# Kernel tuning notes

Hardware: AMD Instinct MI355X
Metric: run time of the kernel (lower is better)

Reference implementation:

```python
import jax, jax.numpy as jnp
import numpy as np

N_HEADS = 4
LN_EPS = 1e-12


def _ln(x, g, b):
    mu = jnp.mean(x, axis=-1, keepdims=True)
    var = jnp.var(x, axis=-1, keepdims=True)
    return (x - mu) * jax.lax.rsqrt(var + LN_EPS) * g + b


def _mha(q_in, kv_in, qkv_w, qkv_b, o_w, o_b):
    # q_in: [B,Sq,H], kv_in: [B,Sk,H]; qkv_w: [3,H,H], qkv_b: [3,H]
    B, Sq, H = q_in.shape
    Sk = kv_in.shape[1]
    hd = H // N_HEADS
    q = (q_in @ qkv_w[0] + qkv_b[0]).reshape(B, Sq, N_HEADS, hd)
    k = (kv_in @ qkv_w[1] + qkv_b[1]).reshape(B, Sk, N_HEADS, hd)
    v = (kv_in @ qkv_w[2] + qkv_b[2]).reshape(B, Sk, N_HEADS, hd)
    scale = 1.0 / jnp.sqrt(jnp.asarray(hd, q_in.dtype))
    scores = jnp.einsum('bqhd,bkhd->bhqk', q, k) * scale  # [B,H,Sq,Sk]
    probs = jax.nn.softmax(scores, axis=-1)
    ctx = jnp.einsum('bhqk,bkhd->bqhd', probs, v).reshape(B, Sq, H)
    return ctx @ o_w + o_b


def reference(x, y, pos_embed, self_qkv_w, self_qkv_b, self_o_w, self_o_b,
              cross_qkv_w, cross_qkv_b, cross_o_w, cross_o_b,
              ffn_w1, ffn_b1, ffn_w2, ffn_b2, ln_g, ln_b):
    # positional embedding added to encoder sequence
    x = x + pos_embed[: x.shape[1]][None]
    h = y
    n_layers = self_qkv_w.shape[0]
    for i in range(n_layers):  # 6 structurally-identical decoder layers
        a = _mha(h, h, self_qkv_w[i], self_qkv_b[i], self_o_w[i], self_o_b[i])
        h = _ln(h + a, ln_g[i, 0], ln_b[i, 0])
        c = _mha(h, x, cross_qkv_w[i], cross_qkv_b[i], cross_o_w[i], cross_o_b[i])
        h = _ln(h + c, ln_g[i, 1], ln_b[i, 1])
        f = jax.nn.gelu(h @ ffn_w1[i] + ffn_b1[i]) @ ffn_w2[i] + ffn_b2[i]
        h = _ln(h + f, ln_g[i, 2], ln_b[i, 2])
    return h


def setup_inputs() -> dict:
    key = jax.random.key(0)
    ks = jax.random.split(key, 12)
    B, Se, Sd, H, L, F = 2, 4096, 2048, 256, 6, 1024
    s = 0.02  # weight init scale
    return {
        'x': jax.random.normal(ks[0], (B, Se, H), jnp.float32),
        'y': jax.random.normal(ks[1], (B, Sd, H), jnp.float32),
        'pos_embed': jax.random.normal(ks[2], (4096, H), jnp.float32) * s,
        'self_qkv_w': jax.random.normal(ks[3], (L, 3, H, H), jnp.float32) * s,
        'self_qkv_b': jnp.zeros((L, 3, H), jnp.float32),
        'self_o_w': jax.random.normal(ks[4], (L, H, H), jnp.float32) * s,
        'self_o_b': jnp.zeros((L, H), jnp.float32),
        'cross_qkv_w': jax.random.normal(ks[5], (L, 3, H, H), jnp.float32) * s,
        'cross_qkv_b': jnp.zeros((L, 3, H), jnp.float32),
        'cross_o_w': jax.random.normal(ks[6], (L, H, H), jnp.float32) * s,
        'cross_o_b': jnp.zeros((L, H), jnp.float32),
        'ffn_w1': jax.random.normal(ks[7], (L, H, F), jnp.float32) * s,
        'ffn_b1': jnp.zeros((L, F), jnp.float32),
        'ffn_w2': jax.random.normal(ks[8], (L, F, H), jnp.float32) * s,
        'ffn_b2': jnp.zeros((L, H), jnp.float32),
        'ln_g': jnp.ones((L, 3, H), jnp.float32),
        'ln_b': jnp.zeros((L, 3, H), jnp.float32),
    }
```

## Files before the change

kernel.cpp:

```cpp
#include <hip/hip_runtime.h>
#include <hip/hip_bf16.h>

typedef unsigned short u16;
typedef __attribute__((ext_vector_type(8))) short bhalf8;
typedef __attribute__((ext_vector_type(4))) short bhalf4;
typedef __attribute__((ext_vector_type(4))) float f32x4;

__device__ inline f32x4 mfma_bf16(bhalf8 a, bhalf8 b, f32x4 c) {
    return __builtin_amdgcn_mfma_f32_16x16x32_bf16(a, b, c, 0, 0, 0);
}
__device__ inline f32x4 mfma16_bf16(bhalf4 a, bhalf4 b, f32x4 c) {
    return __builtin_amdgcn_mfma_f32_16x16x16bf16_1k(a, b, c, 0, 0, 0);
}

__device__ inline u16 f2bf(float f) {
    union { float f; unsigned u; } v; v.f = f;
    unsigned u = v.u;
    return (u16)((u + 0x7fff + ((u >> 16) & 1)) >> 16);
}
__device__ inline unsigned pkbf(float lo_, float hi_) {
    return ((unsigned)f2bf(hi_) << 16) | (unsigned)f2bf(lo_);
}
__device__ inline unsigned pk2bf(float lo, float hi) {
    union { __hip_bfloat162 h; unsigned u; } v;
    v.h = __float22bfloat162_rn(float2{lo, hi});
    return v.u;
}

__device__ inline size_t afm_off(int row, int col, int Cc) {
    return ((size_t)((row >> 4) * Cc + (col >> 5))) * 512
         + (((row & 15) + 16 * ((col >> 3) & 3)) << 3) + (col & 7);
}


__global__ __launch_bounds__(256) void k_wtrans_fm(const float* in, u16* out, int rows, int cols) {
    int mat = blockIdx.y;
    size_t rc = (size_t)rows * cols;
    size_t idx = (size_t)blockIdx.x * 256 + threadIdx.x;
    if (idx >= rc) return;
    int r = (int)(idx / cols), c = (int)(idx % cols);
    size_t off = ((size_t)((c >> 4) * (rows >> 5) + (r >> 5))) * 512
               + (((c & 15) + 16 * ((r >> 3) & 3)) << 3) + (r & 7);
    out[mat * rc + off] = f2bf(in[mat * rc + idx]);
}

__global__ __launch_bounds__(256) void k_addpos(const float* x, const float* pos, u16* xp) {
    size_t idx = (size_t)blockIdx.x * 256 + threadIdx.x;
    size_t p = idx & ((size_t)4096 * 256 - 1);
    int row = (int)(idx >> 8), col = (int)(idx & 255);
    xp[afm_off(row, col, 8)] = f2bf(x[idx] + pos[p]);
}

__global__ __launch_bounds__(256) void k_inith(const float* y, float* h, u16* hb) {
    size_t idx = (size_t)blockIdx.x * 256 + threadIdx.x;
    float v = y[idx];
    h[idx] = v;
    int row = (int)(idx >> 8), col = (int)(idx & 255);
    hb[afm_off(row, col, 8)] = f2bf(v);
}

__global__ __launch_bounds__(256) void k_kv_pre(const u16* A2, const u16* Wall, const float* ball,
                                                u16* kfm_all, u16* vfm_all) {
    const int Skv = 4096;
    int layer = blockIdx.z;
    int wave = threadIdx.x >> 6, lane = threadIdx.x & 63;
    int l16 = lane & 15, quad = lane >> 4;
    int row0 = blockIdx.x * 64 + wave * 16;
    int col0 = blockIdx.y * 32;
    const u16* Wk = Wall + (size_t)layer * 3 * 65536 + 65536;
    const u16* Wv = Wk + 65536;
    const float* bk = ball + layer * 768 + 256;
    const float* bv = bk + 256;
    u16* kout = kfm_all + (size_t)layer * 2097152;
    u16* vout = vfm_all + (size_t)layer * 2097152;
    const int Kc = 8;

    f32x4 acck0 = (f32x4){0.f, 0.f, 0.f, 0.f};
    f32x4 acck1 = (f32x4){0.f, 0.f, 0.f, 0.f};
    f32x4 accv0 = (f32x4){0.f, 0.f, 0.f, 0.f};
    f32x4 accv1 = (f32x4){0.f, 0.f, 0.f, 0.f};
    const u16* ab  = A2 + (size_t)(row0 >> 4) * Kc * 512 + lane * 8;
    const u16* wk0 = Wk + (size_t)(col0 >> 4) * Kc * 512 + lane * 8;
    const u16* wk1 = wk0 + (size_t)Kc * 512;
    const u16* wv0 = Wv + (size_t)(col0 >> 4) * Kc * 512 + lane * 8;
    const u16* wv1 = wv0 + (size_t)Kc * 512;
    #pragma unroll
    for (int kc = 0; kc < Kc; kc++) {
        bhalf8 a = *(const bhalf8*)(ab + kc * 512);
        acck0 = mfma_bf16(a, *(const bhalf8*)(wk0 + kc * 512), acck0);
        acck1 = mfma_bf16(a, *(const bhalf8*)(wk1 + kc * 512), acck1);
        accv0 = mfma_bf16(a, *(const bhalf8*)(wv0 + kc * 512), accv0);
        accv1 = mfma_bf16(a, *(const bhalf8*)(wv1 + kc * 512), accv1);
    }

    {
        f32x4 accs[2] = {acck0, acck1};
        #pragma unroll
        for (int nt = 0; nt < 2; nt++) {
            int col = col0 + nt * 16 + l16;
            float bs = bk[col];
            int hh = col >> 6, dim = col & 63;
            int f = dim >> 5, q8 = (dim >> 3) & 3, i8 = dim & 7;
            #pragma unroll
            for (int r = 0; r < 4; r++) {
                int row = row0 + quad * 4 + r;
                int bb = row / Skv; int key = row - bb * Skv;
                size_t off = (size_t)(bb * 4 + hh) * Skv * 64 + (size_t)(key >> 4) * 1024
                           + f * 512 + q8 * 128 + (key & 15) * 8 + i8;
                kout[off] = f2bf(accs[nt][r] + bs);
            }
        }
    }
    {
        f32x4 accs[2] = {accv0, accv1};
        #pragma unroll
        for (int nt = 0; nt < 2; nt++) {
            int col = col0 + nt * 16 + l16;
            float bs = bv[col];
            int hh = col >> 6, dim = col & 63;
            int ntg = dim >> 4, l16v = dim & 15;
            int row = row0 + quad * 4;
            int bb = row / Skv; int key = row - bb * Skv;
            size_t off = (size_t)(bb * 4 + hh) * Skv * 64 + (size_t)(key >> 4) * 1024
                       + ntg * 256 + ((key & 15) >> 2) * 64 + l16v * 4;
            ushort4 pk;
            pk.x = f2bf(accs[nt][0] + bs);
            pk.y = f2bf(accs[nt][1] + bs);
            pk.z = f2bf(accs[nt][2] + bs);
            pk.w = f2bf(accs[nt][3] + bs);
            *(ushort4*)(vout + off) = pk;
        }
    }
}

__global__ __launch_bounds__(256) void k_gemm_qkv(const u16* A0, const u16* A2,
                                                  const u16* Wfm0, const float* bias0,
                                                  u16* qout, u16* kfm_out, u16* vfm_out,
                                                  int K, long wz, long bz, float scale0,
                                                  int kz, int vz, int Skv, int M0) {
    int z = blockIdx.z;
    int wave = threadIdx.x >> 6, lane = threadIdx.x & 63;
    int l16 = lane & 15, quad = lane >> 4;
    int row0 = blockIdx.x * 64 + wave * 16;
    int col0 = blockIdx.y * 32;
    const u16* A;
    if (z == 0) { if (row0 >= M0) return; A = A0; } else { A = A2; }
    const u16* Wfm = Wfm0 + (size_t)z * wz;
    const float* bias = bias0 + (size_t)z * bz;
    int Kc = K >> 5;

    f32x4 acc0 = (f32x4){0.f, 0.f, 0.f, 0.f};
    f32x4 acc1 = (f32x4){0.f, 0.f, 0.f, 0.f};
    const u16* ab = A + (size_t)(row0 >> 4) * Kc * 512 + lane * 8;
    const u16* wb0 = Wfm + (size_t)(col0 >> 4) * Kc * 512 + lane * 8;
    const u16* wb1 = wb0 + (size_t)Kc * 512;
    #pragma unroll 4
    for (int kc = 0; kc < Kc; kc++) {
        bhalf8 a = *(const bhalf8*)(ab + kc * 512);
        acc0 = mfma_bf16(a, *(const bhalf8*)(wb0 + kc * 512), acc0);
        acc1 = mfma_bf16(a, *(const bhalf8*)(wb1 + kc * 512), acc1);
    }

    f32x4 accs[2] = {acc0, acc1};
    #pragma unroll
    for (int nt = 0; nt < 2; nt++) {
        int col = col0 + nt * 16 + l16;
        float bs = bias[col];
        if (z == kz) {
            int hh = col >> 6, dim = col & 63;
            int f = dim >> 5, q8 = (dim >> 3) & 3, i8 = dim & 7;
            #pragma unroll
            for (int r = 0; r < 4; r++) {
                int row = row0 + quad * 4 + r;
                int bb = row / Skv; int key = row - bb * Skv;
                size_t off = (size_t)(bb * 4 + hh) * Skv * 64 + (size_t)(key >> 4) * 1024
                           + f * 512 + q8 * 128 + (key & 15) * 8 + i8;
                kfm_out[off] = f2bf(accs[nt][r] + bs);
            }
        } else if (z == vz) {
            int hh = col >> 6, dim = col & 63;
            int ntg = dim >> 4, l16v = dim & 15;
            int row = row0 + quad * 4;
            int bb = row / Skv; int key = row - bb * Skv;
            size_t off = (size_t)(bb * 4 + hh) * Skv * 64 + (size_t)(key >> 4) * 1024
                       + ntg * 256 + ((key & 15) >> 2) * 64 + l16v * 4;
            ushort4 pk;
            pk.x = f2bf(accs[nt][0] + bs);
            pk.y = f2bf(accs[nt][1] + bs);
            pk.z = f2bf(accs[nt][2] + bs);
            pk.w = f2bf(accs[nt][3] + bs);
            *(ushort4*)(vfm_out + off) = pk;
        } else {
            size_t base = ((size_t)(row0 >> 4) * 8 + blockIdx.y) * 512;
            int g3 = (nt * 2 + (l16 >> 3)) & 3;
            int i = l16 & 7;
            #pragma unroll
            for (int r = 0; r < 4; r++)
                qout[base + (((quad * 4 + r) + 16 * g3) << 3) + i] =
                    f2bf((accs[nt][r] + bs) * scale0);
        }
    }
}

__global__ __launch_bounds__(512) void k_gemm_ln(const u16* A, const u16* Wfm, const float* bias,
                                                 const float* res, const float* g, const float* beta,
                                                 float* outf, u16* outb, int K) {
    int t = threadIdx.x;
    int w = t >> 6, lane = t & 63;
    int l16 = lane & 15, quad = lane >> 4;
    int row0 = blockIdx.x * 16;
    int Kc = K >> 5;

    f32x4 acc[2];
    acc[0] = (f32x4){0.f, 0.f, 0.f, 0.f};
    acc[1] = (f32x4){0.f, 0.f, 0.f, 0.f};

    const u16* ab = A + (size_t)blockIdx.x * Kc * 512 + lane * 8;
    const u16* wb = Wfm + (size_t)(w * 2) * Kc * 512 + lane * 8;
    #pragma unroll 4
    for (int kc = 0; kc < Kc; kc++) {
        bhalf8 a = *(const bhalf8*)(ab + kc * 512);
        acc[0] = mfma_bf16(a, *(const bhalf8*)(wb + kc * 512), acc[0]);
        acc[1] = mfma_bf16(a, *(const bhalf8*)(wb + (size_t)(Kc + kc) * 512), acc[1]);
    }

    float sr[4] = {0.f, 0.f, 0.f, 0.f}, s2r[4] = {0.f, 0.f, 0.f, 0.f};
    #pragma unroll
    for (int nt = 0; nt < 2; nt++) {
        int col = w * 32 + nt * 16 + l16;
        float bs = bias[col];
        #pragma unroll
        for (int r = 0; r < 4; r++) {
            int row = row0 + quad * 4 + r;
            float v = acc[nt][r] + bs + res[(size_t)row * 256 + col];
            acc[nt][r] = v;
            sr[r] += v; s2r[r] += v * v;
        }
    }
    #pragma unroll
    for (int r = 0; r < 4; r++) {
        #pragma unroll
        for (int off = 8; off >= 1; off >>= 1) {
            sr[r]  += __shfl_xor(sr[r], off, 16);
            s2r[r] += __shfl_xor(s2r[r], off, 16);
        }
    }
    __shared__ float lsm[8][16], lsq[8][16];
    if (l16 == 0) {
        #pragma unroll
        for (int r = 0; r < 4; r++) { lsm[w][quad * 4 + r] = sr[r]; lsq[w][quad * 4 + r] = s2r[r]; }
    }
    __syncthreads();
    float mu[4], rs[4];
    #pragma unroll
    for (int r = 0; r < 4; r++) {
        int ri = quad * 4 + r;
        float ts = 0.f, tq = 0.f;
        #pragma unroll
        for (int ww = 0; ww < 8; ww++) { ts += lsm[ww][ri]; tq += lsq[ww][ri]; }
        mu[r] = ts * (1.f / 256.f);
        float var = tq * (1.f / 256.f) - mu[r] * mu[r];
        rs[r] = rsqrtf(var + 1e-12f);
    }
    size_t base = ((size_t)blockIdx.x * 8 + w) * 512;
    #pragma unroll
    for (int nt = 0; nt < 2; nt++) {
        int col = w * 32 + nt * 16 + l16;
        float gc = g[col], bc = beta[col];
        int g3 = (nt * 2 + (l16 >> 3)) & 3;
        int i = l16 & 7;
        #pragma unroll
        for (int r = 0; r < 4; r++) {
            int row = row0 + quad * 4 + r;
            float yv = (acc[nt][r] - mu[r]) * rs[r] * gc + bc;
            outf[(size_t)row * 256 + col] = yv;
            outb[base + (((quad * 4 + r) + 16 * g3) << 3) + i] = f2bf(yv);
        }
    }
}

__global__ __launch_bounds__(512) void k_ffn(const u16* A, const u16* W1, const float* b1,
                                             const u16* W2, const float* b2,
                                             const float* res, const float* g, const float* beta,
                                             float* outf, u16* outb) {
    int t = threadIdx.x;
    int w = t >> 6, lane = t & 63;
    int l16 = lane & 15, quad = lane >> 4;
    int row0 = blockIdx.x * 16;

    __shared__ u16 f1lds[32 * 512];
    __shared__ float lsm[8][16], lsq[8][16];

    f32x4 acc[8];
    #pragma unroll
    for (int nt = 0; nt < 8; nt++) acc[nt] = (f32x4){0.f, 0.f, 0.f, 0.f};
    const u16* ab = A + (size_t)blockIdx.x * 8 * 512 + lane * 8;
    const u16* w1b = W1 + (size_t)(w * 8) * 8 * 512 + lane * 8;
    #pragma unroll
    for (int kc = 0; kc < 8; kc++) {
        bhalf8 a = *(const bhalf8*)(ab + kc * 512);
        #pragma unroll
        for (int nt = 0; nt < 8; nt++)
            acc[nt] = mfma_bf16(a, *(const bhalf8*)(w1b + ((size_t)nt * 8 + kc) * 512), acc[nt]);
    }
    #pragma unroll
    for (int nt = 0; nt < 8; nt++) {
        int col = w * 128 + nt * 16 + l16;
        float bs = b1[col];
        int chunk = w * 4 + (nt >> 1);
        int g3 = (nt * 2 + (l16 >> 3)) & 3;
        int i = l16 & 7;
        #pragma unroll
        for (int r = 0; r < 4; r++) {
            float v = acc[nt][r] + bs;
            float ge = 0.5f * v * (1.f + tanhf(0.7978845608028654f * (v + 0.044715f * v * v * v)));
            f1lds[chunk * 512 + (((quad * 4 + r) + 16 * g3) << 3) + i] = f2bf(ge);
        }
    }
    __syncthreads();

    f32x4 acc2[2];
    acc2[0] = (f32x4){0.f, 0.f, 0.f, 0.f};
    acc2[1] = (f32x4){0.f, 0.f, 0.f, 0.f};
    const u16* w2b = W2 + (size_t)(w * 2) * 32 * 512 + lane * 8;
    #pragma unroll 4
    for (int kc = 0; kc < 32; kc++) {
        bhalf8 a = *(const bhalf8*)&f1lds[kc * 512 + lane * 8];
        acc2[0] = mfma_bf16(a, *(const bhalf8*)(w2b + (size_t)kc * 512), acc2[0]);
        acc2[1] = mfma_bf16(a, *(const bhalf8*)(w2b + (size_t)(32 + kc) * 512), acc2[1]);
    }

    float sr[4] = {0.f, 0.f, 0.f, 0.f}, s2r[4] = {0.f, 0.f, 0.f, 0.f};
    #pragma unroll
    for (int nt = 0; nt < 2; nt++) {
        int col = w * 32 + nt * 16 + l16;
        float bs = b2[col];
        #pragma unroll
        for (int r = 0; r < 4; r++) {
            int row = row0 + quad * 4 + r;
            float v = acc2[nt][r] + bs + res[(size_t)row * 256 + col];
            acc2[nt][r] = v;
            sr[r] += v; s2r[r] += v * v;
        }
    }
    #pragma unroll
    for (int r = 0; r < 4; r++) {
        #pragma unroll
        for (int off = 8; off >= 1; off >>= 1) {
            sr[r]  += __shfl_xor(sr[r], off, 16);
            s2r[r] += __shfl_xor(s2r[r], off, 16);
        }
    }
    if (l16 == 0) {
        #pragma unroll
        for (int r = 0; r < 4; r++) { lsm[w][quad * 4 + r] = sr[r]; lsq[w][quad * 4 + r] = s2r[r]; }
    }
    __syncthreads();
    float mu[4], rs[4];
    #pragma unroll
    for (int r = 0; r < 4; r++) {
        int ri = quad * 4 + r;
        float ts = 0.f, tq = 0.f;
        #pragma unroll
        for (int ww = 0; ww < 8; ww++) { ts += lsm[ww][ri]; tq += lsq[ww][ri]; }
        mu[r] = ts * (1.f / 256.f);
        float var = tq * (1.f / 256.f) - mu[r] * mu[r];
        rs[r] = rsqrtf(var + 1e-12f);
    }
    size_t base = ((size_t)blockIdx.x * 8 + w) * 512;
    #pragma unroll
    for (int nt = 0; nt < 2; nt++) {
        int col = w * 32 + nt * 16 + l16;
        float gc = g[col], bc = beta[col];
        int g3 = (nt * 2 + (l16 >> 3)) & 3;
        int i = l16 & 7;
        #pragma unroll
        for (int r = 0; r < 4; r++) {
            int row = row0 + quad * 4 + r;
            float yv = (acc2[nt][r] - mu[r]) * rs[r] * gc + bc;
            outf[(size_t)row * 256 + col] = yv;
            outb[base + (((quad * 4 + r) + 16 * g3) << 3) + i] = f2bf(yv);
        }
    }
}

__global__ __launch_bounds__(512, 4) void k_attn(const u16* q, const u16* kfm, const u16* vfm,
                                                 u16* ctx, int Sq, int Sk) {
    int bh = blockIdx.x & 7;
    int b = bh >> 2, h = bh & 3;
    int qp = blockIdx.x >> 3;
    int t = threadIdx.x;
    int kw = t >> 6, lane = t & 63;
    int l16 = lane & 15, quad = lane >> 4;
    int q0 = qp * 32;

    __shared__ float opart[2][7][64][20];
    __shared__ float lsum[2][7][16];

    size_t rt0 = (size_t)((b * Sq + q0) >> 4);
    const u16* qb = q + (rt0 * 8 + h * 2) * 512 + lane * 8;
    bhalf8 bq00 = *(const bhalf8*)(qb);
    bhalf8 bq01 = *(const bhalf8*)(qb + 512);
    bhalf8 bq10 = *(const bhalf8*)(qb + 8 * 512);
    bhalf8 bq11 = *(const bhalf8*)(qb + 9 * 512);

    const u16* kwb = kfm + (size_t)(b * 4 + h) * Sk * 64;
    const u16* vwb = vfm + (size_t)(b * 4 + h) * Sk * 64;

    int nT = Sk >> 7;
    int T0 = kw * nT;

    float l0 = 0.f, l1 = 0.f;
    f32x4 o0[4], o1[4];
    #pragma unroll
    for (int nt = 0; nt < 4; nt++) {
        o0[nt] = (f32x4){0.f, 0.f, 0.f, 0.f};
        o1[nt] = (f32x4){0.f, 0.f, 0.f, 0.f};
    }

    #pragma unroll 2
    for (int T = T0; T < T0 + nT; T++) {
        const u16* kt = kwb + (size_t)T * 1024;
        bhalf8 a0 = *(const bhalf8*)(kt + lane * 8);
        bhalf8 a1 = *(const bhalf8*)(kt + 512 + lane * 8);
        f32x4 s0 = (f32x4){0.f, 0.f, 0.f, 0.f};
        f32x4 s1 = (f32x4){0.f, 0.f, 0.f, 0.f};
        s0 = mfma_bf16(a0, bq00, s0);
        s0 = mfma_bf16(a1, bq01, s0);
        s1 = mfma_bf16(a0, bq10, s1);
        s1 = mfma_bf16(a1, bq11, s1);

        float p0[4], p1[4], ps0 = 0.f, ps1 = 0.f;
        #pragma unroll
        for (int r = 0; r < 4; r++) {
            p0[r] = exp2f(s0[r] - 11.5415603f);
            ps0 += p0[r];
            p1[r] = exp2f(s1[r] - 11.5415603f);
            ps1 += p1[r];
        }
        l0 += ps0; l1 += ps1;

        union { bhalf4 v; unsigned u[2]; } bp0, bp1;
        bp0.u[0] = pk2bf(p0[0], p0[1]);
        bp0.u[1] = pk2bf(p0[2], p0[3]);
        bp1.u[0] = pk2bf(p1[0], p1[1]);
        bp1.u[1] = pk2bf(p1[2], p1[3]);

        const u16* vts = vwb + (size_t)T * 1024 + quad * 64 + l16 * 4;
        #pragma unroll
        for (int nt = 0; nt < 4; nt++) {
            bhalf4 va = *(const bhalf4*)(vts + nt * 256);
            o0[nt] = mfma16_bf16(va, bp0.v, o0[nt]);
            o1[nt] = mfma16_bf16(va, bp1.v, o1[nt]);
        }
    }

    float lc0 = l0, lc1 = l1;
    lc0 += __shfl_xor(lc0, 16, 64);
    lc0 += __shfl_xor(lc0, 32, 64);
    lc1 += __shfl_xor(lc1, 16, 64);
    lc1 += __shfl_xor(lc1, 32, 64);

    if (kw > 0) {
        #pragma unroll
        for (int nt = 0; nt < 4; nt++)
            #pragma unroll
            for (int r = 0; r < 4; r++) {
                opart[0][kw - 1][nt * 16 + quad * 4 + r][l16] = o0[nt][r];
                opart[1][kw - 1][nt * 16 + quad * 4 + r][l16] = o1[nt][r];
            }
        if (quad == 0) {
            lsum[0][kw - 1][l16] = lc0;
            lsum[1][kw - 1][l16] = lc1;
        }
    }
    __syncthreads();
    if (kw == 0) {
        float L0 = lc0, L1 = lc1;
        #pragma unroll
        for (int ww = 0; ww < 7; ww++) {
            L0 += lsum[0][ww][l16];
            L1 += lsum[1][ww][l16];
        }
        float invL0 = 1.f / L0;
        float invL1 = 1.f / L1;
        #pragma unroll
        for (int nt = 0; nt < 4; nt++) {
            ushort4 pkv0, pkv1;
            #pragma unroll
            for (int r = 0; r < 4; r++) {
                float v0 = o0[nt][r];
                float v1 = o1[nt][r];
                #pragma unroll
                for (int ww = 0; ww < 7; ww++) {
                    v0 += opart[0][ww][nt * 16 + quad * 4 + r][l16];
                    v1 += opart[1][ww][nt * 16 + quad * 4 + r][l16];
                }
                ((u16*)&pkv0)[r] = f2bf(v0 * invL0);
                ((u16*)&pkv1)[r] = f2bf(v1 * invL1);
            }
            size_t ce = ((l16 + 16 * ((nt * 2 + (quad >> 1)) & 3)) << 3) + (quad & 1) * 4;
            size_t off0 = (rt0 * 8 + (h * 2 + (nt >> 1))) * 512 + ce;
            size_t off1 = ((rt0 + 1) * 8 + (h * 2 + (nt >> 1))) * 512 + ce;
            *(ushort4*)(ctx + off0) = pkv0;
            *(ushort4*)(ctx + off1) = pkv1;
        }
    }
}

extern "C" void kernel_launch(void* const* d_in, const int* in_sizes, int n_in,
                              void* d_out, int out_size, void* d_ws, size_t ws_size,
                              hipStream_t stream) {
    const float* x        = (const float*)d_in[0];
    const float* y        = (const float*)d_in[1];
    const float* pos      = (const float*)d_in[2];
    const float* sqkv_w   = (const float*)d_in[3];
    const float* sqkv_b   = (const float*)d_in[4];
    const float* so_w     = (const float*)d_in[5];
    const float* so_b     = (const float*)d_in[6];
    const float* cqkv_w   = (const float*)d_in[7];
    const float* cqkv_b   = (const float*)d_in[8];
    const float* co_w     = (const float*)d_in[9];
    const float* co_b     = (const float*)d_in[10];
    const float* ffn_w1   = (const float*)d_in[11];
    const float* ffn_b1   = (const float*)d_in[12];
    const float* ffn_w2   = (const float*)d_in[13];
    const float* ffn_b2   = (const float*)d_in[14];
    const float* ln_g     = (const float*)d_in[15];
    const float* ln_b     = (const float*)d_in[16];

    char* w = (char*)d_ws;
    auto alloc = [&](size_t bytes) { char* p = w; w += (bytes + 255) & ~(size_t)255; return p; };

    u16* wt_sqkv = (u16*)alloc(18ull * 65536 * 2);
    u16* wt_so   = (u16*)alloc(6ull  * 65536 * 2);
    u16* wt_cqkv = (u16*)alloc(18ull * 65536 * 2);
    u16* wt_co   = (u16*)alloc(6ull  * 65536 * 2);
    u16* wt_f1   = (u16*)alloc(6ull  * 262144 * 2);
    u16* wt_f2   = (u16*)alloc(6ull  * 262144 * 2);
    u16* xp      = (u16*)alloc(2097152ull * 2);
    float* hf    = (float*)alloc(1048576ull * 4);
    u16* hb      = (u16*)alloc(1048576ull * 2);
    u16* qbuf    = (u16*)alloc(1048576ull * 2);
    u16* kfm     = (u16*)alloc(2097152ull * 2);
    u16* vfm     = (u16*)alloc(2097152ull * 2);
    u16* ctx     = (u16*)alloc(1048576ull * 2);
    u16* kfm_all = (u16*)alloc(6ull * 2097152 * 2);
    u16* vfm_all = (u16*)alloc(6ull * 2097152 * 2);

    k_wtrans_fm<<<dim3(256, 18), 256, 0, stream>>>(sqkv_w, wt_sqkv, 256, 256);
    k_wtrans_fm<<<dim3(256, 6),  256, 0, stream>>>(so_w,   wt_so,   256, 256);
    k_wtrans_fm<<<dim3(256, 18), 256, 0, stream>>>(cqkv_w, wt_cqkv, 256, 256);
    k_wtrans_fm<<<dim3(256, 6),  256, 0, stream>>>(co_w,   wt_co,   256, 256);
    k_wtrans_fm<<<dim3(1024, 6), 256, 0, stream>>>(ffn_w1, wt_f1,   256, 1024);
    k_wtrans_fm<<<dim3(1024, 6), 256, 0, stream>>>(ffn_w2, wt_f2,   1024, 256);
    k_addpos<<<dim3(8192), 256, 0, stream>>>(x, pos, xp);
    k_inith<<<dim3(4096), 256, 0, stream>>>(y, hf, hb);
    k_kv_pre<<<dim3(128, 8, 6), 256, 0, stream>>>(xp, wt_cqkv, cqkv_b, kfm_all, vfm_all);

    const float qscale = 0.125f * 1.44269504f;

    for (int i = 0; i < 6; i++) {
        k_gemm_qkv<<<dim3(64, 8, 3), 256, 0, stream>>>(hb, hb,
            wt_sqkv + (size_t)i * 3 * 65536, sqkv_b + i * 768,
            qbuf, kfm, vfm, 256, 65536, 256, qscale, 1, 2, 2048, 4096);
        k_attn<<<dim3(512), 512, 0, stream>>>(qbuf, kfm, vfm, ctx, 2048, 2048);
        k_gemm_ln<<<dim3(256), 512, 0, stream>>>(ctx, wt_so + (size_t)i * 65536,
            so_b + i * 256, hf, ln_g + (i * 3 + 0) * 256, ln_b + (i * 3 + 0) * 256,
            hf, hb, 256);

        k_gemm_qkv<<<dim3(64, 8, 1), 256, 0, stream>>>(hb, xp,
            wt_cqkv + (size_t)i * 3 * 65536, cqkv_b + i * 768,
            qbuf, kfm, vfm, 256, 65536, 256, qscale, 1, 2, 4096, 4096);
        k_attn<<<dim3(512), 512, 0, stream>>>(qbuf,
            kfm_all + (size_t)i * 2097152, vfm_all + (size_t)i * 2097152, ctx, 2048, 4096);
        k_gemm_ln<<<dim3(256), 512, 0, stream>>>(ctx, wt_co + (size_t)i * 65536,
            co_b + i * 256, hf, ln_g + (i * 3 + 1) * 256, ln_b + (i * 3 + 1) * 256,
            hf, hb, 256);

        float* dst = (i == 5) ? (float*)d_out : hf;
        k_ffn<<<dim3(256), 512, 0, stream>>>(hb, wt_f1 + (size_t)i * 262144,
            ffn_b1 + i * 1024, wt_f2 + (size_t)i * 262144, ffn_b2 + i * 256,
            hf, ln_g + (i * 3 + 2) * 256, ln_b + (i * 3 + 2) * 256, dst, hb);
    }
}
```

Before: 863.7 us.

## Stage cross-attention K/V weights in LDS and enlarge k_kv_pre tiles

The precompute kernel for cross-attention K/V now loads a 64-column slice of the K and V weights into shared memory once per block. Each block then iterates over 4 row tiles of 64 rows and 2 column pairs, with A fragments held in registers. This replaces the earlier direct global loads of weights per 16x32 tile and cuts redundant weight traffic. The cost is 64KB of LDS per block and a 4x smaller grid, which lowers occupancy and parallelism in a kernel that runs only once.

```diff
diff --git a/kernel.cpp b/kernel.cpp
--- a/kernel.cpp
+++ b/kernel.cpp
@@ -65,8 +65,6 @@
     int layer = blockIdx.z;
     int wave = threadIdx.x >> 6, lane = threadIdx.x & 63;
     int l16 = lane & 15, quad = lane >> 4;
-    int row0 = blockIdx.x * 64 + wave * 16;
-    int col0 = blockIdx.y * 32;
     const u16* Wk = Wall + (size_t)layer * 3 * 65536 + 65536;
     const u16* Wv = Wk + 65536;
     const float* bk = ball + layer * 768 + 256;
@@ -75,60 +73,82 @@
     u16* vout = vfm_all + (size_t)layer * 2097152;
     const int Kc = 8;
 
-    f32x4 acck0 = (f32x4){0.f, 0.f, 0.f, 0.f};
-    f32x4 acck1 = (f32x4){0.f, 0.f, 0.f, 0.f};
-    f32x4 accv0 = (f32x4){0.f, 0.f, 0.f, 0.f};
-    f32x4 accv1 = (f32x4){0.f, 0.f, 0.f, 0.f};
-    const u16* ab  = A2 + (size_t)(row0 >> 4) * Kc * 512 + lane * 8;
-    const u16* wk0 = Wk + (size_t)(col0 >> 4) * Kc * 512 + lane * 8;
-    const u16* wk1 = wk0 + (size_t)Kc * 512;
-    const u16* wv0 = Wv + (size_t)(col0 >> 4) * Kc * 512 + lane * 8;
-    const u16* wv1 = wv0 + (size_t)Kc * 512;
-    #pragma unroll
-    for (int kc = 0; kc < Kc; kc++) {
-        bhalf8 a = *(const bhalf8*)(ab + kc * 512);
-        acck0 = mfma_bf16(a, *(const bhalf8*)(wk0 + kc * 512), acck0);
-        acck1 = mfma_bf16(a, *(const bhalf8*)(wk1 + kc * 512), acck1);
-        accv0 = mfma_bf16(a, *(const bhalf8*)(wv0 + kc * 512), accv0);
-        accv1 = mfma_bf16(a, *(const bhalf8*)(wv1 + kc * 512), accv1);
-    }
-
-    {
-        f32x4 accs[2] = {acck0, acck1};
-        #pragma unroll
-        for (int nt = 0; nt < 2; nt++) {
-            int col = col0 + nt * 16 + l16;
-            float bs = bk[col];
-            int hh = col >> 6, dim = col & 63;
-            int f = dim >> 5, q8 = (dim >> 3) & 3, i8 = dim & 7;
+    __shared__ u16 wlds[8 * 4096];
+    #pragma unroll
+    for (int c = 0; c < 8; c++) {
+        int cp = c >> 2, mat = (c >> 1) & 1, nt = c & 1;
+        const u16* s = (mat ? Wv : Wk)
+                     + (size_t)(((blockIdx.y * 64 + cp * 32) >> 4) + nt) * 4096;
+        *(bhalf8*)&wlds[c * 4096 + threadIdx.x * 16]     = *(const bhalf8*)(s + threadIdx.x * 16);
+        *(bhalf8*)&wlds[c * 4096 + threadIdx.x * 16 + 8] = *(const bhalf8*)(s + threadIdx.x * 16 + 8);
+    }
+    __syncthreads();
+
+    for (int rt = 0; rt < 4; rt++) {
+        int row0 = blockIdx.x * 256 + rt * 64 + wave * 16;
+        const u16* ab = A2 + (size_t)(row0 >> 4) * Kc * 512 + lane * 8;
+        bhalf8 af[8];
+        #pragma unroll
+        for (int kc = 0; kc < 8; kc++) af[kc] = *(const bhalf8*)(ab + kc * 512);
+
+        #pragma unroll
+        for (int cp = 0; cp < 2; cp++) {
+            int col0 = blockIdx.y * 64 + cp * 32;
+            const u16* lk0 = &wlds[(cp * 4 + 0) * 4096 + lane * 8];
+            const u16* lk1 = &wlds[(cp * 4 + 1) * 4096 + lane * 8];
+            const u16* lv0 = &wlds[(cp * 4 + 2) * 4096 + lane * 8];
+            const u16* lv1 = &wlds[(cp * 4 + 3) * 4096 + lane * 8];
+            f32x4 acck0 = (f32x4){0.f, 0.f, 0.f, 0.f};
+            f32x4 acck1 = (f32x4){0.f, 0.f, 0.f, 0.f};
+            f32x4 accv0 = (f32x4){0.f, 0.f, 0.f, 0.f};
+            f32x4 accv1 = (f32x4){0.f, 0.f, 0.f, 0.f};
             #pragma unroll
-            for (int r = 0; r < 4; r++) {
-                int row = row0 + quad * 4 + r;
-                int bb = row / Skv; int key = row - bb * Skv;
-                size_t off = (size_t)(bb * 4 + hh) * Skv * 64 + (size_t)(key >> 4) * 1024
-                           + f * 512 + q8 * 128 + (key & 15) * 8 + i8;
-                kout[off] = f2bf(accs[nt][r] + bs);
+            for (int kc = 0; kc < Kc; kc++) {
+                bhalf8 a = af[kc];
+                acck0 = mfma_bf16(a, *(const bhalf8*)(lk0 + kc * 512), acck0);
+                acck1 = mfma_bf16(a, *(const bhalf8*)(lk1 + kc * 512), acck1);
+                accv0 = mfma_bf16(a, *(const bhalf8*)(lv0 + kc * 512), accv0);
+                accv1 = mfma_bf16(a, *(const bhalf8*)(lv1 + kc * 512), accv1);
             }
-        }
-    }
-    {
-        f32x4 accs[2] = {accv0, accv1};
-        #pragma unroll
-        for (int nt = 0; nt < 2; nt++) {
-            int col = col0 + nt * 16 + l16;
-            float bs = bv[col];
-            int hh = col >> 6, dim = col & 63;
-            int ntg = dim >> 4, l16v = dim & 15;
-            int row = row0 + quad * 4;
-            int bb = row / Skv; int key = row - bb * Skv;
-            size_t off = (size_t)(bb * 4 + hh) * Skv * 64 + (size_t)(key >> 4) * 1024
-                       + ntg * 256 + ((key & 15) >> 2) * 64 + l16v * 4;
-            ushort4 pk;
-            pk.x = f2bf(accs[nt][0] + bs);
-            pk.y = f2bf(accs[nt][1] + bs);
-            pk.z = f2bf(accs[nt][2] + bs);
-            pk.w = f2bf(accs[nt][3] + bs);
-            *(ushort4*)(vout + off) = pk;
+
+            {
+                f32x4 accs[2] = {acck0, acck1};
+                #pragma unroll
+                for (int nt = 0; nt < 2; nt++) {
+                    int col = col0 + nt * 16 + l16;
+                    float bs = bk[col];
+                    int hh = col >> 6, dim = col & 63;
+                    int f = dim >> 5, q8 = (dim >> 3) & 3, i8 = dim & 7;
+                    #pragma unroll
+                    for (int r = 0; r < 4; r++) {
+                        int row = row0 + quad * 4 + r;
+                        int bb = row / Skv; int key = row - bb * Skv;
+                        size_t off = (size_t)(bb * 4 + hh) * Skv * 64 + (size_t)(key >> 4) * 1024
+                                   + f * 512 + q8 * 128 + (key & 15) * 8 + i8;
+                        kout[off] = f2bf(accs[nt][r] + bs);
+                    }
+                }
+            }
+            {
+                f32x4 accs[2] = {accv0, accv1};
+                #pragma unroll
+                for (int nt = 0; nt < 2; nt++) {
+                    int col = col0 + nt * 16 + l16;
+                    float bs = bv[col];
+                    int hh = col >> 6, dim = col & 63;
+                    int ntg = dim >> 4, l16v = dim & 15;
+                    int row = row0 + quad * 4;
+                    int bb = row / Skv; int key = row - bb * Skv;
+                    size_t off = (size_t)(bb * 4 + hh) * Skv * 64 + (size_t)(key >> 4) * 1024
+                               + ntg * 256 + ((key & 15) >> 2) * 64 + l16v * 4;
+                    ushort4 pk;
+                    pk.x = f2bf(accs[nt][0] + bs);
+                    pk.y = f2bf(accs[nt][1] + bs);
+                    pk.z = f2bf(accs[nt][2] + bs);
+                    pk.w = f2bf(accs[nt][3] + bs);
+                    *(ushort4*)(vout + off) = pk;
+                }
+            }
         }
     }
 }
@@ -556,7 +576,7 @@
     k_wtrans_fm<<<dim3(1024, 6), 256, 0, stream>>>(ffn_w2, wt_f2,   1024, 256);
     k_addpos<<<dim3(8192), 256, 0, stream>>>(x, pos, xp);
     k_inith<<<dim3(4096), 256, 0, stream>>>(y, hf, hb);
-    k_kv_pre<<<dim3(128, 8, 6), 256, 0, stream>>>(xp, wt_cqkv, cqkv_b, kfm_all, vfm_all);
+    k_kv_pre<<<dim3(32, 4, 6), 256, 0, stream>>>(xp, wt_cqkv, cqkv_b, kfm_all, vfm_all);
 
     const float qscale = 0.125f * 1.44269504f;
 
```

Result: no change. 864.1 us (+0.1%).
